# Kernel optimization log

Measured on AMD Instinct MI355X. Metric: run time of the kernel, lower is better.

The kernel has to match this reference:

```python
import jax, jax.numpy as jnp
import numpy as np

N = 2048
DIM = 1024
NH = 16
DK = DIM // NH  # 64

def setup_inputs() -> dict:
    key = jax.random.key(0)
    kx, kq, kk, kv = jax.random.split(key, 4)
    # nn.Linear(dim_in, dim_in, bias=False): init ~ U(-1/sqrt(dim_in), 1/sqrt(dim_in))
    b = 1.0 / np.sqrt(DIM)
    return {
        "x": jax.random.normal(kx, (N, DIM), dtype=jnp.float32),
        "rela": jnp.zeros((1,), dtype=jnp.float32),  # unused by the module
        "Wq": jax.random.uniform(kq, (DIM, DIM), jnp.float32, -b, b),
        "Wk": jax.random.uniform(kk, (DIM, DIM), jnp.float32, -b, b),
        "Wv": jax.random.uniform(kv, (DIM, DIM), jnp.float32, -b, b),
    }

def reference(x, rela, Wq, Wk, Wv):
    n = x.shape[0]
    scale = 1.0 / np.sqrt(DK)
    # torch Linear: x @ W.T ; reshape to [n, nh, dk] then heads first -> [nh, n, dk]
    q = (x @ Wq.T).reshape(n, NH, DK).transpose(1, 0, 2)
    k = (x @ Wk.T).reshape(n, NH, DK).transpose(1, 0, 2)
    v = (x @ Wv.T).reshape(n, NH, DK).transpose(1, 0, 2)
    dist = jnp.einsum('hnd,hmd->hnm', q, k) * scale  # [nh, n, n]
    dist = jax.nn.softmax(dist, axis=-1)
    att = jnp.einsum('hnm,hmd->hnd', dist, v)        # [nh, n, dk]
    return att.transpose(1, 0, 2).reshape(n, DIM)
```

## Files before the change

### kernel.cpp

```cpp
#include <hip/hip_runtime.h>

#define SN 2048
#define SDIM 1024
#define SNH 16
#define SDK 64

typedef short short8 __attribute__((ext_vector_type(8)));
typedef short s16x4 __attribute__((ext_vector_type(4)));
typedef unsigned short u16;
typedef u16 u16x4 __attribute__((ext_vector_type(4)));
typedef unsigned u32x4 __attribute__((ext_vector_type(4)));
typedef float f32x4 __attribute__((ext_vector_type(4)));

__device__ __forceinline__ u16 f2b(float f){
  unsigned u = __builtin_bit_cast(unsigned, f);
  u += 0x7fffu + ((u >> 16) & 1u);
  return (u16)(u >> 16);
}

__device__ __forceinline__ float b2f(u16 b){
  unsigned u = ((unsigned)b) << 16;
  return __builtin_bit_cast(float, u);
}

__device__ __forceinline__ float fast_exp2(float x){
#if __has_builtin(__builtin_amdgcn_exp2f)
  return __builtin_amdgcn_exp2f(x);
#else
  float r; asm("v_exp_f32 %0, %1" : "=v"(r) : "v"(x)); return r;
#endif
}

__device__ __forceinline__ void async_cp16(const void* g, void* l){
  __builtin_amdgcn_global_load_lds(
      (const __attribute__((address_space(1))) unsigned*)g,
      (__attribute__((address_space(3))) unsigned*)l, 16, 0, 0);
}

__global__ void conv_all(const float* __restrict__ x, const float* __restrict__ wq,
                         const float* __restrict__ wk, const float* __restrict__ wv,
                         u16* __restrict__ xb, u16* __restrict__ wb){
  const int NX4 = (SN * SDIM) / 4;
  const int NW4 = (SDIM * SDIM) / 4;
  const int total = NX4 + 3 * NW4;
  int i = blockIdx.x * blockDim.x + threadIdx.x;
  int stride = gridDim.x * blockDim.x;
  for (int idx = i; idx < total; idx += stride){
    const float* src; u16* dst; int off;
    if (idx < NX4){ src = x; dst = xb; off = idx; }
    else {
      int t = idx - NX4; int ws = t >> 18; off = t & (NW4 - 1);
      src = (ws == 0) ? wq : ((ws == 1) ? wk : wv);
      dst = wb + (size_t)ws * SDIM * SDIM;
    }
    float4 v = reinterpret_cast<const float4*>(src)[off];
    u16x4 o = { f2b(v.x), f2b(v.y), f2b(v.z), f2b(v.w) };
    *reinterpret_cast<u16x4*>(&dst[(size_t)off * 4]) = o;
  }
}

__global__ __launch_bounds__(512, 6) void proj_gemm(const u16* __restrict__ xb, const u16* __restrict__ wb,
                                                    u16* __restrict__ qb, u16* __restrict__ kb,
                                                    u16* __restrict__ vtb){
  __shared__ __align__(16) u16 Asm[2][64 * 64];
  __shared__ __align__(16) u16 Bsm[2][128 * 64];
  const int tid = threadIdx.x, w = tid >> 6, lane = tid & 63;
  const int r = lane & 15, hi = lane >> 4;
  const int tm = blockIdx.x * 64, tn = blockIdx.y * 128;
  const int z = blockIdx.z;
  const u16* W = wb + (size_t)z * SDIM * SDIM;
  const int kk = w >> 2;
  const int wr = (w >> 1) & 1, wc = w & 1;
  const int srow = lane >> 3;
  const int schunk = (lane & 7) ^ (lane >> 3);
  f32x4 acc[2][4] = {};

  auto stage = [&](int b, int kt){
    async_cp16(xb + (size_t)(tm + w * 8 + srow) * SDIM + kt + schunk * 8, &Asm[b][w * 8 * 64]);
#pragma unroll
    for (int c = 0; c < 2; c++){
      int row = w * 16 + c * 8;
      async_cp16(W + (size_t)(tn + row + srow) * SDIM + kt + schunk * 8, &Bsm[b][row * 64]);
    }
  };

  stage(0, 0);
  asm volatile("s_waitcnt vmcnt(0)" ::: "memory");
  __builtin_amdgcn_s_barrier();
  __builtin_amdgcn_sched_barrier(0);

  int cur = 0;
  for (int kt = 0; kt < SDIM; kt += 64){
    if (kt + 64 < SDIM) stage(cur ^ 1, kt + 64);
    __builtin_amdgcn_s_setprio(1);
    {
      short8 af[2], bf[4];
      int cc = (kk * 4 + hi) ^ (r & 7);
#pragma unroll
      for (int mr = 0; mr < 2; mr++)
        af[mr] = *reinterpret_cast<const short8*>(&Asm[cur][(wr * 32 + mr * 16 + r) * 64 + cc * 8]);
#pragma unroll
      for (int nr = 0; nr < 4; nr++)
        bf[nr] = *reinterpret_cast<const short8*>(&Bsm[cur][(wc * 64 + nr * 16 + r) * 64 + cc * 8]);
#pragma unroll
      for (int mr = 0; mr < 2; mr++)
#pragma unroll
        for (int nr = 0; nr < 4; nr++)
          acc[mr][nr] = __builtin_amdgcn_mfma_f32_16x16x32_bf16(af[mr], bf[nr], acc[mr][nr], 0, 0, 0);
    }
    __builtin_amdgcn_s_setprio(0);
    asm volatile("s_waitcnt vmcnt(0)" ::: "memory");
    __builtin_amdgcn_s_barrier();
    __builtin_amdgcn_sched_barrier(0);
    cur ^= 1;
  }

  float* scr = reinterpret_cast<float*>(&Bsm[0][0]);
  const int slot = w & 3;
  if (kk == 1){
#pragma unroll
    for (int mr = 0; mr < 2; mr++)
#pragma unroll
      for (int nr = 0; nr < 4; nr++){
        int fid = mr * 4 + nr;
        int a = slot * 2048 + fid * 256 + r * 16 + ((hi + r) & 3) * 4;
        *reinterpret_cast<f32x4*>(&scr[a]) = acc[mr][nr];
      }
  }
  __syncthreads();
  if (kk == 0){
#pragma unroll
    for (int mr = 0; mr < 2; mr++)
#pragma unroll
      for (int nr = 0; nr < 4; nr++){
        int fid = mr * 4 + nr;
        int a = slot * 2048 + fid * 256 + r * 16 + ((hi + r) & 3) * 4;
        f32x4 t = *reinterpret_cast<const f32x4*>(&scr[a]);
        acc[mr][nr][0] += t[0]; acc[mr][nr][1] += t[1];
        acc[mr][nr][2] += t[2]; acc[mr][nr][3] += t[3];
      }

    if (z == 2){
#pragma unroll
      for (int mr = 0; mr < 2; mr++)
#pragma unroll
        for (int nr = 0; nr < 4; nr++){
          u16x4 o4 = { f2b(acc[mr][nr][0]), f2b(acc[mr][nr][1]),
                       f2b(acc[mr][nr][2]), f2b(acc[mr][nr][3]) };
          int col = tn + wc * 64 + nr * 16 + r;
          int row = tm + wr * 32 + mr * 16 + hi * 4;
          *reinterpret_cast<u16x4*>(&vtb[(size_t)col * SN + row]) = o4;
        }
    } else {
      u16* outp = (z == 0) ? qb : kb;
      const float scl = (z == 0) ? 0.18033688011112043f : 1.0f;
#pragma unroll
      for (int mr = 0; mr < 2; mr++)
#pragma unroll
        for (int nr = 0; nr < 4; nr++)
#pragma unroll
          for (int j = 0; j < 4; j++){
            int row = tm + wr * 32 + mr * 16 + hi * 4 + j;
            int col = tn + wc * 64 + nr * 16 + r;
            outp[(size_t)row * SDIM + col] = f2b(acc[mr][nr][j] * scl);
          }
    }
  }
}

__global__ __launch_bounds__(256, 3) void attn(const u16* __restrict__ qb, const u16* __restrict__ kb,
                                               const u16* __restrict__ vtb,
                                               u16* __restrict__ po, float* __restrict__ pl){
  __shared__ __align__(16) u16 klds[2][64 * 64];
  __shared__ __align__(16) u16 vlds[2][64 * 64];
  const int tid = threadIdx.x, w = tid >> 6, lane = tid & 63;
  const int r = lane & 15, hi = lane >> 4;

  int flat = blockIdx.x + 16 * blockIdx.y + 256 * blockIdx.z;
  int sw = (flat & 7) * 128 + (flat >> 3);
  const int q0 = (sw & 15) * 128, h = (sw >> 4) & 15, z = sw >> 8;

  const int srow_off = lane >> 3;
  const int schunk   = (lane & 7) ^ (lane >> 3);

  short8 aq[2][2];
#pragma unroll
  for (int sub = 0; sub < 2; sub++){
    int qrow = q0 + w * 32 + sub * 16 + r;
    aq[sub][0] = *reinterpret_cast<const short8*>(&qb[(size_t)qrow * SDIM + h * SDK + hi * 8]);
    aq[sub][1] = *reinterpret_cast<const short8*>(&qb[(size_t)qrow * SDIM + h * SDK + 32 + hi * 8]);
  }
  f32x4 oacc[2][4] = {};
  float lacc0 = 0.f, lacc1 = 0.f;

  auto stage = [&](int b, int t){
#pragma unroll
    for (int c = 0; c < 2; c++){
      int rho = w * 16 + c * 8 + srow_off;
      int kvp = 32 * (rho >> 5) + 8 * ((rho >> 2) & 3) + 4 * ((rho >> 4) & 1) + (rho & 3);
      async_cp16(kb  + (size_t)(t + kvp) * SDIM + h * SDK + schunk * 8,
                 &klds[b][(w * 16 + c * 8) * 64]);
      int row = rho;
      async_cp16(vtb + (size_t)(h * SDK + row) * SN + t + schunk * 8,
                 &vlds[b][(w * 16 + c * 8) * 64]);
    }
  };

  const int t0 = z * (SN / 4), tend = t0 + (SN / 4);
  stage(0, t0);
  asm volatile("s_waitcnt vmcnt(0)" ::: "memory");
  __builtin_amdgcn_s_barrier();
  __builtin_amdgcn_sched_barrier(0);

  int cur = 0;
  for (int t = t0; t < tend; t += 64){
    if (t + 64 < tend) stage(cur ^ 1, t + 64);

    const u16* kbuf = &klds[cur][0];
    const u16* vbuf = &vlds[cur][0];

    f32x4 s0[4], s1[4];
    __builtin_amdgcn_s_setprio(1);
#pragma unroll
    for (int ct = 0; ct < 4; ct++){
      int row = ct * 16 + r;
      int c0 = hi ^ (r & 7);
      short8 bk0 = *reinterpret_cast<const short8*>(&kbuf[row * 64 + c0 * 8]);
      short8 bk1 = *reinterpret_cast<const short8*>(&kbuf[row * 64 + (c0 ^ 4) * 8]);
      f32x4 zero = {};
      s0[ct] = __builtin_amdgcn_mfma_f32_16x16x32_bf16(bk0, aq[0][0], zero, 0, 0, 0);
      s1[ct] = __builtin_amdgcn_mfma_f32_16x16x32_bf16(bk0, aq[1][0], zero, 0, 0, 0);
      s0[ct] = __builtin_amdgcn_mfma_f32_16x16x32_bf16(bk1, aq[0][1], s0[ct], 0, 0, 0);
      s1[ct] = __builtin_amdgcn_mfma_f32_16x16x32_bf16(bk1, aq[1][1], s1[ct], 0, 0, 0);
    }
    __builtin_amdgcn_s_setprio(0);

    uint2 pc0[4], pc1[4];
#pragma unroll
    for (int ct = 0; ct < 4; ct++){
      float a0 = fast_exp2(s0[ct][0]), a1 = fast_exp2(s0[ct][1]);
      float a2 = fast_exp2(s0[ct][2]), a3 = fast_exp2(s0[ct][3]);
      lacc0 += (a0 + a1) + (a2 + a3);
      pc0[ct].x = (__builtin_bit_cast(unsigned, a0) >> 16) |
                  (__builtin_bit_cast(unsigned, a1) & 0xffff0000u);
      pc0[ct].y = (__builtin_bit_cast(unsigned, a2) >> 16) |
                  (__builtin_bit_cast(unsigned, a3) & 0xffff0000u);
      float b0 = fast_exp2(s1[ct][0]), b1 = fast_exp2(s1[ct][1]);
      float b2 = fast_exp2(s1[ct][2]), b3 = fast_exp2(s1[ct][3]);
      lacc1 += (b0 + b1) + (b2 + b3);
      pc1[ct].x = (__builtin_bit_cast(unsigned, b0) >> 16) |
                  (__builtin_bit_cast(unsigned, b1) & 0xffff0000u);
      pc1[ct].y = (__builtin_bit_cast(unsigned, b2) >> 16) |
                  (__builtin_bit_cast(unsigned, b3) & 0xffff0000u);
    }
    short8 paf0[2], paf1[2];
#pragma unroll
    for (int c = 0; c < 2; c++){
      u32x4 u0 = { pc0[2*c].x, pc0[2*c].y, pc0[2*c+1].x, pc0[2*c+1].y };
      u32x4 u1 = { pc1[2*c].x, pc1[2*c].y, pc1[2*c+1].x, pc1[2*c+1].y };
      paf0[c] = __builtin_bit_cast(short8, u0);
      paf1[c] = __builtin_bit_cast(short8, u1);
    }

    __builtin_amdgcn_s_setprio(1);
#pragma unroll
    for (int dt = 0; dt < 4; dt++){
      int row = dt * 16 + r;
      int swz = row & 7;
      short8 bvc[2];
#pragma unroll
      for (int c = 0; c < 2; c++)
        bvc[c] = *reinterpret_cast<const short8*>(&vbuf[row * 64 + ((4 * c + hi) ^ swz) * 8]);
#pragma unroll
      for (int c = 0; c < 2; c++){
        oacc[0][dt] = __builtin_amdgcn_mfma_f32_16x16x32_bf16(paf0[c], bvc[c], oacc[0][dt], 0, 0, 0);
        oacc[1][dt] = __builtin_amdgcn_mfma_f32_16x16x32_bf16(paf1[c], bvc[c], oacc[1][dt], 0, 0, 0);
      }
    }
    __builtin_amdgcn_s_setprio(0);

    asm volatile("s_waitcnt vmcnt(0)" ::: "memory");
    __builtin_amdgcn_s_barrier();
    __builtin_amdgcn_sched_barrier(0);
    cur ^= 1;
  }

  lacc0 += __shfl_xor(lacc0, 16); lacc0 += __shfl_xor(lacc0, 32);
  lacc1 += __shfl_xor(lacc1, 16); lacc1 += __shfl_xor(lacc1, 32);

  const size_t zh = (size_t)z * SNH + h;
#pragma unroll
  for (int sub = 0; sub < 2; sub++)
#pragma unroll
    for (int dt = 0; dt < 4; dt++)
#pragma unroll
      for (int j = 0; j < 4; j++){
        int row = q0 + w * 32 + sub * 16 + hi * 4 + j;
        po[(zh * SN + row) * SDK + dt * 16 + r] = f2b(oacc[sub][dt][j]);
      }
  if (hi == 0){
    pl[zh * SN + q0 + w * 32 + r] = lacc0;
    pl[zh * SN + q0 + w * 32 + 16 + r] = lacc1;
  }
}

__global__ void merge(const u16* __restrict__ po, const float* __restrict__ pl,
                      float* __restrict__ out){
  int gid = blockIdx.x * blockDim.x + threadIdx.x;
  int c4 = gid & 15;
  int rowid = gid >> 4;
  int h = rowid & 15, q = rowid >> 4;
  float L = 0.f;
  float4 o = { 0.f, 0.f, 0.f, 0.f };
#pragma unroll
  for (int z = 0; z < 4; z++){
    size_t zh = (size_t)z * SNH + h;
    L += pl[zh * SN + q];
    u16x4 a = *reinterpret_cast<const u16x4*>(&po[(zh * SN + q) * SDK + c4 * 4]);
    o.x += b2f(a[0]); o.y += b2f(a[1]); o.z += b2f(a[2]); o.w += b2f(a[3]);
  }
  float rL = 1.0f / L;
  o.x *= rL; o.y *= rL; o.z *= rL; o.w *= rL;
  reinterpret_cast<float4*>(&out[(size_t)q * SDIM + h * SDK])[c4] = o;
}

extern "C" void kernel_launch(void* const* d_in, const int* in_sizes, int n_in,
                              void* d_out, int out_size, void* d_ws, size_t ws_size,
                              hipStream_t stream){
  const float* x  = (const float*)d_in[0];
  const float* Wq = (const float*)d_in[2];
  const float* Wk = (const float*)d_in[3];
  const float* Wv = (const float*)d_in[4];
  float* out = (float*)d_out;

  char* ws = (char*)d_ws;
  u16* xb  = (u16*)(ws);
  u16* wb  = (u16*)(ws + (4  << 20));
  u16* qb  = (u16*)(ws + (10 << 20));
  u16* kb  = (u16*)(ws + (14 << 20));
  u16* vtb = (u16*)(ws + (18 << 20));
  u16* po  = (u16*)(ws + (22 << 20));
  float* pl = (float*)(ws + (38 << 20));

  conv_all<<<2048, 256, 0, stream>>>(x, Wq, Wk, Wv, xb, wb);

  dim3 pg(SN / 64, SDIM / 128, 3);
  proj_gemm<<<pg, 512, 0, stream>>>(xb, wb, qb, kb, vtb);

  dim3 ag(SN / 128, SNH, 4);
  attn<<<ag, 256, 0, stream>>>(qb, kb, vtb, po, pl);

  merge<<<(SN * SNH * 16) / 256, 256, 0, stream>>>(po, pl, out);
}
```

Measured before the change: 60.15 us.

## Fuse split-K merge into attention via last-arriver atomic counter

Drops the separate merge kernel. Each attention block now increments an atomic counter for its (head, query-tile) group, and the fourth block to finish reads all partial outputs and row sums and writes the normalized result. The counters are zeroed in the conversion kernel. Block-index remapping keeps the four z-splits of a group on the same XCD so partials stay in shared L2. The aim is to save a kernel launch and its tail, at the cost of a serialized tail merge inside some blocks plus a fence and an atomic per block.

After: 206.7 us. +243.7%, slower.

```diff
diff --git a/kernel.cpp b/kernel.cpp
--- a/kernel.cpp
+++ b/kernel.cpp
@@ -39,7 +39,8 @@
 
 __global__ void conv_all(const float* __restrict__ x, const float* __restrict__ wq,
                          const float* __restrict__ wk, const float* __restrict__ wv,
-                         u16* __restrict__ xb, u16* __restrict__ wb){
+                         u16* __restrict__ xb, u16* __restrict__ wb, int* __restrict__ cnt){
+  if (blockIdx.x == 0 && threadIdx.x < 256) cnt[threadIdx.x] = 0;
   const int NX4 = (SN * SDIM) / 4;
   const int NW4 = (SDIM * SDIM) / 4;
   const int total = NX4 + 3 * NW4;
@@ -170,15 +171,20 @@
 
 __global__ __launch_bounds__(256, 3) void attn(const u16* __restrict__ qb, const u16* __restrict__ kb,
                                                const u16* __restrict__ vtb,
-                                               u16* __restrict__ po, float* __restrict__ pl){
+                                               u16* __restrict__ po, float* __restrict__ pl,
+                                               float* __restrict__ out, int* __restrict__ cnt){
   __shared__ __align__(16) u16 klds[2][64 * 64];
   __shared__ __align__(16) u16 vlds[2][64 * 64];
+  __shared__ float Lr[128];
+  __shared__ int tailflag;
   const int tid = threadIdx.x, w = tid >> 6, lane = tid & 63;
   const int r = lane & 15, hi = lane >> 4;
 
   int flat = blockIdx.x + 16 * blockIdx.y + 256 * blockIdx.z;
-  int sw = (flat & 7) * 128 + (flat >> 3);
-  const int q0 = (sw & 15) * 128, h = (sw >> 4) & 15, z = sw >> 8;
+  const int xcd = flat & 7, idx = flat >> 3;
+  const int g = xcd * 32 + (idx & 31);
+  const int z = idx >> 5;
+  const int q0 = (g & 15) * 128, h = g >> 4;
 
   const int srow_off = lane >> 3;
   const int schunk   = (lane & 7) ^ (lane >> 3);
@@ -200,8 +206,7 @@
       int kvp = 32 * (rho >> 5) + 8 * ((rho >> 2) & 3) + 4 * ((rho >> 4) & 1) + (rho & 3);
       async_cp16(kb  + (size_t)(t + kvp) * SDIM + h * SDK + schunk * 8,
                  &klds[b][(w * 16 + c * 8) * 64]);
-      int row = rho;
-      async_cp16(vtb + (size_t)(h * SDK + row) * SN + t + schunk * 8,
+      async_cp16(vtb + (size_t)(h * SDK + rho) * SN + t + schunk * 8,
                  &vlds[b][(w * 16 + c * 8) * 64]);
     }
   };
@@ -302,26 +307,37 @@
     pl[zh * SN + q0 + w * 32 + r] = lacc0;
     pl[zh * SN + q0 + w * 32 + 16 + r] = lacc1;
   }
-}
-
-__global__ void merge(const u16* __restrict__ po, const float* __restrict__ pl,
-                      float* __restrict__ out){
-  int gid = blockIdx.x * blockDim.x + threadIdx.x;
-  int c4 = gid & 15;
-  int rowid = gid >> 4;
-  int h = rowid & 15, q = rowid >> 4;
-  float L = 0.f;
-  float4 o = { 0.f, 0.f, 0.f, 0.f };
-#pragma unroll
-  for (int z = 0; z < 4; z++){
-    size_t zh = (size_t)z * SNH + h;
-    L += pl[zh * SN + q];
-    u16x4 a = *reinterpret_cast<const u16x4*>(&po[(zh * SN + q) * SDK + c4 * 4]);
-    o.x += b2f(a[0]); o.y += b2f(a[1]); o.z += b2f(a[2]); o.w += b2f(a[3]);
-  }
-  float rL = 1.0f / L;
-  o.x *= rL; o.y *= rL; o.z *= rL; o.w *= rL;
-  reinterpret_cast<float4*>(&out[(size_t)q * SDIM + h * SDK])[c4] = o;
+
+  __threadfence();
+  __syncthreads();
+  if (tid == 0){
+    int old = __hip_atomic_fetch_add(&cnt[g], 1, __ATOMIC_ACQ_REL, __HIP_MEMORY_SCOPE_AGENT);
+    tailflag = (old == 3);
+  }
+  __syncthreads();
+  if (tailflag){
+    if (tid < 128){
+      float L = 0.f;
+#pragma unroll
+      for (int z2 = 0; z2 < 4; z2++)
+        L += pl[((size_t)z2 * SNH + h) * SN + q0 + tid];
+      Lr[tid] = 1.0f / L;
+    }
+    __syncthreads();
+    for (int i = tid; i < 2048; i += 256){
+      int row = i >> 4, c4 = i & 15;
+      float4 o = { 0.f, 0.f, 0.f, 0.f };
+#pragma unroll
+      for (int z2 = 0; z2 < 4; z2++){
+        u16x4 a = *reinterpret_cast<const u16x4*>(
+            &po[(((size_t)z2 * SNH + h) * SN + q0 + row) * SDK + c4 * 4]);
+        o.x += b2f(a[0]); o.y += b2f(a[1]); o.z += b2f(a[2]); o.w += b2f(a[3]);
+      }
+      float rL = Lr[row];
+      o.x *= rL; o.y *= rL; o.z *= rL; o.w *= rL;
+      *reinterpret_cast<float4*>(&out[(size_t)(q0 + row) * SDIM + h * SDK + c4 * 4]) = o;
+    }
+  }
 }
 
 extern "C" void kernel_launch(void* const* d_in, const int* in_sizes, int n_in,
@@ -341,14 +357,13 @@
   u16* vtb = (u16*)(ws + (18 << 20));
   u16* po  = (u16*)(ws + (22 << 20));
   float* pl = (float*)(ws + (38 << 20));
-
-  conv_all<<<2048, 256, 0, stream>>>(x, Wq, Wk, Wv, xb, wb);
+  int* cnt = (int*)(ws + (39 << 20));
+
+  conv_all<<<2048, 256, 0, stream>>>(x, Wq, Wk, Wv, xb, wb, cnt);
 
   dim3 pg(SN / 64, SDIM / 128, 3);
   proj_gemm<<<pg, 512, 0, stream>>>(xb, wb, qb, kb, vtb);
 
   dim3 ag(SN / 128, SNH, 4);
-  attn<<<ag, 256, 0, stream>>>(qb, kb, vtb, po, pl);
-
-  merge<<<(SN * SNH * 16) / 256, 256, 0, stream>>>(po, pl, out);
-}
+  attn<<<ag, 256, 0, stream>>>(qb, kb, vtb, po, pl, out, cnt);
+}
```

## Software-pipeline attention loop: overlap next QK^T with current PV

Applied to the files above, without the earlier changes.

Restructures the split-K attention inner loop into a software pipeline. K loads are split from V loads and K is prefetched two tiles ahead, while the QK^T MFMAs for tile i+1 are issued alongside the PV MFMAs for tile i, followed by exp/pack. The goal is to hide exp and VALU latency behind matrix work and to separate the K and V load timing. The cost is extra live registers for the s0/s1 and paf values, which may lower occupancy or cause spills.

After: 60.61 us. No clear change (+0.8%).

```diff
diff --git a/kernel.cpp b/kernel.cpp
--- a/kernel.cpp
+++ b/kernel.cpp
@@ -192,34 +192,27 @@
   }
   f32x4 oacc[2][4] = {};
   float lacc0 = 0.f, lacc1 = 0.f;
-
-  auto stage = [&](int b, int t){
+  short8 paf0[2], paf1[2];
+
+  auto stageK = [&](int buf, int t){
 #pragma unroll
     for (int c = 0; c < 2; c++){
       int rho = w * 16 + c * 8 + srow_off;
       int kvp = 32 * (rho >> 5) + 8 * ((rho >> 2) & 3) + 4 * ((rho >> 4) & 1) + (rho & 3);
-      async_cp16(kb  + (size_t)(t + kvp) * SDIM + h * SDK + schunk * 8,
-                 &klds[b][(w * 16 + c * 8) * 64]);
-      int row = rho;
-      async_cp16(vtb + (size_t)(h * SDK + row) * SN + t + schunk * 8,
-                 &vlds[b][(w * 16 + c * 8) * 64]);
-    }
-  };
-
-  const int t0 = z * (SN / 4), tend = t0 + (SN / 4);
-  stage(0, t0);
-  asm volatile("s_waitcnt vmcnt(0)" ::: "memory");
-  __builtin_amdgcn_s_barrier();
-  __builtin_amdgcn_sched_barrier(0);
-
-  int cur = 0;
-  for (int t = t0; t < tend; t += 64){
-    if (t + 64 < tend) stage(cur ^ 1, t + 64);
-
-    const u16* kbuf = &klds[cur][0];
-    const u16* vbuf = &vlds[cur][0];
-
-    f32x4 s0[4], s1[4];
+      async_cp16(kb + (size_t)(t + kvp) * SDIM + h * SDK + schunk * 8,
+                 &klds[buf][(w * 16 + c * 8) * 64]);
+    }
+  };
+  auto stageV = [&](int buf, int t){
+#pragma unroll
+    for (int c = 0; c < 2; c++){
+      int rho = w * 16 + c * 8 + srow_off;
+      async_cp16(vtb + (size_t)(h * SDK + rho) * SN + t + schunk * 8,
+                 &vlds[buf][(w * 16 + c * 8) * 64]);
+    }
+  };
+
+  auto QK = [&](const u16* kbuf, f32x4* s0, f32x4* s1){
     __builtin_amdgcn_s_setprio(1);
 #pragma unroll
     for (int ct = 0; ct < 4; ct++){
@@ -234,7 +227,9 @@
       s1[ct] = __builtin_amdgcn_mfma_f32_16x16x32_bf16(bk1, aq[1][1], s1[ct], 0, 0, 0);
     }
     __builtin_amdgcn_s_setprio(0);
-
+  };
+
+  auto EXPPACK = [&](const f32x4* s0, const f32x4* s1){
     uint2 pc0[4], pc1[4];
 #pragma unroll
     for (int ct = 0; ct < 4; ct++){
@@ -253,7 +248,6 @@
       pc1[ct].y = (__builtin_bit_cast(unsigned, b2) >> 16) |
                   (__builtin_bit_cast(unsigned, b3) & 0xffff0000u);
     }
-    short8 paf0[2], paf1[2];
 #pragma unroll
     for (int c = 0; c < 2; c++){
       u32x4 u0 = { pc0[2*c].x, pc0[2*c].y, pc0[2*c+1].x, pc0[2*c+1].y };
@@ -261,7 +255,9 @@
       paf0[c] = __builtin_bit_cast(short8, u0);
       paf1[c] = __builtin_bit_cast(short8, u1);
     }
-
+  };
+
+  auto PV = [&](const u16* vbuf){
     __builtin_amdgcn_s_setprio(1);
 #pragma unroll
     for (int dt = 0; dt < 4; dt++){
@@ -278,11 +274,36 @@
       }
     }
     __builtin_amdgcn_s_setprio(0);
-
+  };
+
+  const int t0 = z * (SN / 4);
+  const int NT = (SN / 4) / 64;
+
+  stageK(0, t0); stageV(0, t0); stageK(1, t0 + 64);
+  asm volatile("s_waitcnt vmcnt(0)" ::: "memory");
+  __builtin_amdgcn_s_barrier();
+  __builtin_amdgcn_sched_barrier(0);
+  {
+    f32x4 s0[4], s1[4];
+    QK(&klds[0][0], s0, s1);
+    EXPPACK(s0, s1);
+  }
+  __builtin_amdgcn_s_barrier();
+  __builtin_amdgcn_sched_barrier(0);
+
+  for (int it = 0; it < NT; ++it){
+    const int cur = it & 1;
+    const int t = t0 + it * 64;
+    const bool hasN1 = (it + 1 < NT), hasN2 = (it + 2 < NT);
+    if (hasN1) stageV(cur ^ 1, t + 64);
+    if (hasN2) stageK(cur, t + 128);
+    f32x4 s0[4], s1[4];
+    if (hasN1) QK(&klds[cur ^ 1][0], s0, s1);
+    PV(&vlds[cur][0]);
+    if (hasN1) EXPPACK(s0, s1);
     asm volatile("s_waitcnt vmcnt(0)" ::: "memory");
     __builtin_amdgcn_s_barrier();
     __builtin_amdgcn_sched_barrier(0);
-    cur ^= 1;
   }
 
   lacc0 += __shfl_xor(lacc0, 16); lacc0 += __shfl_xor(lacc0, 32);
```
